# Performance work log

Measured on AMD Instinct MI355X. Metric: run time of the kernel, lower is better.

## Reference

```python
import jax, jax.numpy as jnp
import numpy as np

PI = float(np.pi)
BN_EPS = 1e-3
LN_EPS = 1e-5


def ssslu(x, shape, bias):
    # x * (sin(softsign(x) * shape*pi/2) + (bias + 1))
    s = x / (1.0 + jnp.abs(x))
    return x * (jnp.sin(s * (shape * PI / 2.0)) + (bias + 1.0))


def bn(x, g, b, m, v):
    inv = (g / jnp.sqrt(v + BN_EPS))[None, :, None, None]
    return (x - m[None, :, None, None]) * inv + b[None, :, None, None]


def conv2d(x, w, bias=None, pad=0):
    y = jax.lax.conv_general_dilated(x, w, (1, 1), [(pad, pad), (pad, pad)],
                                     dimension_numbers=('NCHW', 'OIHW', 'NCHW'))
    if bias is not None:
        y = y + bias[None, :, None, None]
    return y


def ln_silu(v):
    # LayerNorm (unit weight, zero bias) over last axis, then SiLU
    mu = jnp.mean(v, axis=-1, keepdims=True)
    var = jnp.mean(jnp.square(v - mu), axis=-1, keepdims=True)
    h = (v - mu) / jnp.sqrt(var + LN_EPS)
    return h * jax.nn.sigmoid(h)


def _forward(x, w_qkv, g_qkv, b_qkv, m_qkv, v_qkv,
             w_co, g_co, b_co, m_co, v_co,
             w_b1, bias_b1, g_b1, b_b1, m_b1, v_b1,
             w_b2, bias_b2, g_b2, b_b2, m_b2, v_b2):
    B, C, H, W = x.shape
    Q = (w_qkv.shape[0] - C) // 2
    # qkv Conv block: conv1x1 -> SSSLU(-3, 0.3) -> BN
    t = bn(ssslu(conv2d(x, w_qkv, pad=0), -3.0, 0.3), g_qkv, b_qkv, m_qkv, v_qkv)
    xq, xk, xv = jnp.split(t, [Q, 2 * Q], axis=1)
    # max-pooled Q/K rows and columns -> [B*Q, W] / [B*Q, H]
    qw = jnp.max(xq, axis=2).reshape(B * Q, W)
    kw = jnp.max(xk, axis=2).reshape(B * Q, W)
    qh = jnp.max(xq, axis=3).reshape(B * Q, H)
    kh = jnp.max(xk, axis=3).reshape(B * Q, H)
    # xaw[i,b] = max_a qw[i,a]*kw[i,b]; xah[i,a] = max_b qh[i,a]*kh[i,b]
    xaw = jnp.max(qw[:, :, None] * kw[:, None, :], axis=1)  # [BQ, W]
    xah = jnp.max(qh[:, :, None] * kh[:, None, :], axis=2)  # [BQ, H]
    xaw = ln_silu(xaw)
    xah = ln_silu(xah)
    xa = (xah[:, :, None] * xaw[:, None, :]).reshape(B, Q, H, W)
    # co: SSSLUConv(Q+C -> Q): conv3x3 -> BN -> SSSLU(1.0, 0)
    xa = jnp.concatenate([xa, xv], axis=1)
    xa = ssslu(bn(conv2d(xa, w_co, pad=1), g_co, b_co, m_co, v_co), 1.0, 0.0)
    # back[0]: Conv(Q -> C, k3, bias): conv -> SSSLU(-3, 0.3) -> BN
    xa = bn(ssslu(conv2d(xa, w_b1, bias_b1, pad=1), -3.0, 0.3), g_b1, b_b1, m_b1, v_b1)
    # back[1]: SSSLUConv(C -> C, k1, bias): conv -> BN -> SSSLU(0.8, 0)
    xa = ssslu(bn(conv2d(xa, w_b2, bias_b2, pad=0), g_b2, b_b2, m_b2, v_b2), 0.8, 0.0)
    # back[2]: Sigmoid; source returns the gate itself
    return jax.nn.sigmoid(xa)


def setup_inputs() -> dict:
    B, C, Q, H, W = 16, 256, 256, 64, 64
    key = jax.random.key(0)
    ks = jax.random.split(key, 32)

    def w_init(k, o, i, kh, kw):
        return jax.random.normal(k, (o, i, kh, kw), jnp.float32) * (1.0 / np.sqrt(i * kh * kw))

    def bn_params(k, c):
        k1, k2, k3, k4 = jax.random.split(k, 4)
        g = jax.random.uniform(k1, (c,), jnp.float32, 0.5, 1.5)
        b = jax.random.normal(k2, (c,), jnp.float32) * 0.1
        m = jax.random.normal(k3, (c,), jnp.float32) * 0.1
        v = jax.random.uniform(k4, (c,), jnp.float32, 0.5, 1.5)
        return g, b, m, v

    x = jax.random.normal(ks[0], (B, C, H, W), jnp.float32)
    w_qkv = w_init(ks[1], 2 * Q + C, C, 1, 1)
    g_qkv, b_qkv, m_qkv, v_qkv = bn_params(ks[2], 2 * Q + C)
    w_co = w_init(ks[3], Q, Q + C, 3, 3)
    g_co, b_co, m_co, v_co = bn_params(ks[4], Q)
    w_b1 = w_init(ks[5], C, Q, 3, 3)
    bias_b1 = jax.random.normal(ks[6], (C,), jnp.float32) * 0.05
    g_b1, b_b1, m_b1, v_b1 = bn_params(ks[7], C)
    w_b2 = w_init(ks[8], C, C, 1, 1)
    bias_b2 = jax.random.normal(ks[9], (C,), jnp.float32) * 0.05
    g_b2, b_b2, m_b2, v_b2 = bn_params(ks[10], C)
    return dict(x=x, w_qkv=w_qkv, g_qkv=g_qkv, b_qkv=b_qkv, m_qkv=m_qkv, v_qkv=v_qkv,
                w_co=w_co, g_co=g_co, b_co=b_co, m_co=m_co, v_co=v_co,
                w_b1=w_b1, bias_b1=bias_b1, g_b1=g_b1, b_b1=b_b1, m_b1=m_b1, v_b1=v_b1,
                w_b2=w_b2, bias_b2=bias_b2, g_b2=g_b2, b_b2=b_b2, m_b2=m_b2, v_b2=v_b2)


def reference(x, w_qkv, g_qkv, b_qkv, m_qkv, v_qkv,
              w_co, g_co, b_co, m_co, v_co,
              w_b1, bias_b1, g_b1, b_b1, m_b1, v_b1,
              w_b2, bias_b2, g_b2, b_b2, m_b2, v_b2):
    return _forward(x, w_qkv, g_qkv, b_qkv, m_qkv, v_qkv,
                    w_co, g_co, b_co, m_co, v_co,
                    w_b1, bias_b1, g_b1, b_b1, m_b1, v_b1,
                    w_b2, bias_b2, g_b2, b_b2, m_b2, v_b2)
```

## Files before the change

### kernel.cpp

```cpp
#include <hip/hip_runtime.h>
#include <hip/hip_bf16.h>
#include <math.h>

#define PI_F 3.14159265358979323846f

typedef unsigned short u16;
typedef unsigned int   u32;
typedef float    f32x4 __attribute__((ext_vector_type(4)));
typedef _Float16 f16x8 __attribute__((ext_vector_type(8)));
typedef u16      u16x8 __attribute__((ext_vector_type(8)));
typedef u16      u16x4 __attribute__((ext_vector_type(4)));

__device__ __forceinline__ u16 f2h(float f){ union{ _Float16 h; u16 u; } c; c.h = (_Float16)f; return c.u; }
__device__ __forceinline__ float h2f(u16 u){ union{ u16 u; _Float16 h; } c; c.u = u; return (float)c.h; }

__device__ __forceinline__ void gl16(const void* g, void* l){
  __builtin_amdgcn_global_load_lds((const __attribute__((address_space(1))) u32*)g,
                                   (__attribute__((address_space(3))) u32*)l, 16, 0, 0);
}

__device__ __forceinline__ int SWZ(int r){ return (r>>1)&3; }

__device__ __forceinline__ float wred_max(float v){
#pragma unroll
  for (int m = 32; m; m >>= 1) v = fmaxf(v, __shfl_xor(v, m));
  return v;
}
__device__ __forceinline__ float wred_min(float v){
#pragma unroll
  for (int m = 32; m; m >>= 1) v = fminf(v, __shfl_xor(v, m));
  return v;
}
__device__ __forceinline__ float wred_sum(float v){
#pragma unroll
  for (int m = 32; m; m >>= 1) v += __shfl_xor(v, m);
  return v;
}

__device__ __forceinline__ float ssslu_f(float x, float shp, float bp1){
  float s = x / (1.0f + fabsf(x));
  return x * (__sinf(s * shp) + bp1);
}

__device__ __forceinline__ float epi_val(float v, float4 p, float shp, float bp1, int ORDER, bool SIG){
  v += p.w;
  if (ORDER == 0){ v = ssslu_f(v, shp, bp1); v = (v - p.z) * p.x + p.y; }
  else           { v = (v - p.z) * p.x + p.y; v = ssslu_f(v, shp, bp1); }
  if (SIG) v = 1.f / (1.f + __expf(-v));
  return v;
}

__device__ __forceinline__ f16x8 mul8h(u16x8 a, u16x8 b){
  union{ u16x8 u; f16x8 h; } A, B; A.u = a; B.u = b;
  return A.h * B.h;
}

__global__ __launch_bounds__(256)
void xpose_k(const float* __restrict__ X, u16* __restrict__ XH)
{
  __shared__ u16 L[16384];
  const int tid = threadIdx.x;
  const int b = blockIdx.x >> 6, h = blockIdx.x & 63;
  const float* xp = X + (size_t)b * 256 * 4096 + h * 64;
#pragma unroll
  for (int i = 0; i < 16; ++i){
    int ci = i * 16 + (tid >> 4);
    int w4 = (tid & 15) * 4;
    float4 v = *(const float4*)(xp + (size_t)ci * 4096 + w4);
    int sw = 4 * ((ci >> 3) & 15);
    u16x4 d;
    d[0] = f2h(v.x); d[1] = f2h(v.y); d[2] = f2h(v.z); d[3] = f2h(v.w);
    *(u16x4*)&L[ci * 64 + (w4 ^ sw)] = d;
  }
  __syncthreads();
  u16* out = XH + (((size_t)b * 4096 + (size_t)h * 64) << 8);
#pragma unroll
  for (int it = 0; it < 8; ++it){
    int w   = it * 8 + (tid >> 5);
    int m   = tid & 31;
    int ci0 = m * 8;
    int base = (w & ~3) ^ (4 * (m & 15));
    int wl   = w & 3;
    u16x8 o;
#pragma unroll
    for (int k = 0; k < 8; ++k)
      o[k] = L[(ci0 + k) * 64 + base + wl];
    *(u16x8*)&out[w * 256 + ci0] = o;
  }
}

template<int CI_T, bool CAT>
__global__ __launch_bounds__(256, 2)
void conv3_mfma(const u16* __restrict__ Apk, const u16* __restrict__ Bg,
                u16* __restrict__ DstH, const float4* __restrict__ pp,
                const u16* __restrict__ xahT_, const u16* __restrict__ xawT_,
                float shp, float bp1, int ORDER)
{
  constexpr int NCC = CI_T / 32;
  constexpr int NIT = NCC * 3;
  __shared__ __align__(16) u16 sAB[37248];

  const int tid  = threadIdx.x;
  const int lane = tid & 63;
  const int wv   = tid >> 6;
  const int wn   = wv;
  const int l15  = lane & 15, l4 = lane >> 4;

  const int bx  = blockIdx.x;
  const int bid = (bx & 7) * 32 + (bx >> 3);
  const int b   = bid >> 4;
  const int r0  = (bid & 15) * 4;
  const int m0  = blockIdx.y * 128;

  if (tid < 192){
    int rr = tid >> 5, rem = tid & 31;
    int wp = (rem & 16) ? 65 : 0;
    *(u32*)&sAB[24576 + rr * 2112 + wp * 32 + (rem & 15) * 2] = 0;
  }
  if (r0 == 0)
    for (int i = tid; i < 1056; i += 256) *(u32*)&sAB[24576 + i * 2] = 0;
  if (r0 == 60)
    for (int i = tid; i < 1056; i += 256) *(u32*)&sAB[24576 + 5 * 2112 + i * 2] = 0;

  const int rA = tid >> 2, s4 = tid & 3;
  const u32 offA0 = ((u32)rA * CI_T + ((s4 ^ SWZ(rA)) << 3)) * 2;
  const u32 offA1 = ((u32)(rA + 64) * CI_T + ((s4 ^ SWZ(rA + 64)) << 3)) * 2;
  const u32 offB  = (((u32)rA << 8) + ((s4 ^ SWZ(rA + 1)) << 3)) * 2;

  auto STAGE_A = [&](int it2){
    int d2 = it2 % 3, c2 = it2 / 3;
    u16* dst = &sAB[(it2 & 1) * 12288 + wv * 512];
    const char* pa = (const char*)(Apk + ((size_t)(d2 * 3 * 256) + m0) * CI_T + c2 * 32);
#pragma unroll
    for (int j2 = 0; j2 < 3; ++j2){
      gl16(pa + offA0, dst + j2 * 4096);
      gl16(pa + offA1, dst + j2 * 4096 + 2048);
      pa += (size_t)256 * CI_T * 2;
    }
  };
  auto STAGE_B = [&](int c2){
#pragma unroll
    for (int j = 0; j < 6; ++j){
      int hh = r0 - 1 + j;
      if ((unsigned)hh >= 64u) continue;
      if (CAT && c2 < 8){
        int w = rA, s = s4;
        int ci0 = c2 * 32 + ((s ^ SWZ(w + 1)) << 3);
        u16x8 vh = *(const u16x8*)&xahT_[((b * 64 + hh) << 8) + ci0];
        u16x8 vw = *(const u16x8*)&xawT_[((b * 64 + w ) << 8) + ci0];
        *(f16x8*)&sAB[24576 + j * 2112 + (w + 1) * 32 + s * 8] = mul8h(vh, vw);
      } else {
        int cio = CAT ? (c2 * 32 - 256) : (c2 * 32);
        const char* pb = (const char*)(Bg + (((size_t)b * 4096 + (size_t)hh * 64) << 8) + cio);
        gl16(pb + offB, &sAB[24576 + j * 2112 + 32 + wv * 512]);
      }
    }
  };

  f32x4 acc[8][4];
#pragma unroll
  for (int i = 0; i < 8; ++i)
#pragma unroll
    for (int j = 0; j < 4; ++j){ acc[i][j][0]=0.f; acc[i][j][1]=0.f; acc[i][j][2]=0.f; acc[i][j][3]=0.f; }

  const char* lds = (const char*)sAB;
  const u32 aoff = (u32)l15 * 64 + (u32)((l4 ^ ((l15 >> 1) & 3)) << 4);
  const char* ab0 = lds + aoff;
  const char* ab1 = lds + aoff + 24576;
  const u32 bcom = 49152u + (u32)wn * 4224;
  const char* bb0 = lds + bcom + (u32)(l15 + 0) * 64 + (u32)((l4 ^ (((l15 + 0) >> 1) & 3)) << 4);
  const char* bb1 = lds + bcom + (u32)(l15 + 1) * 64 + (u32)((l4 ^ (((l15 + 1) >> 1) & 3)) << 4);
  const char* bb2 = lds + bcom + (u32)(l15 + 2) * 64 + (u32)((l4 ^ (((l15 + 2) >> 1) & 3)) << 4);

  STAGE_A(0);

  for (int c = 0; c < NCC; ++c){
#pragma unroll
    for (int d = 0; d < 3; ++d){
      const int it = 3 * c + d;
      if (it + 1 < NIT) STAGE_A(it + 1);
      if (d == 0){ STAGE_B(c); __syncthreads(); }

      const char* ab = ((c + d) & 1) ? ab1 : ab0;
#pragma unroll
      for (int dw = 0; dw < 3; ++dw){
        const char* bp = (dw == 0) ? bb0 : (dw == 1) ? bb1 : bb2;
        f16x8 afr[8], bfr[4];
#pragma unroll
        for (int fm = 0; fm < 8; ++fm)
          afr[fm] = *(const f16x8*)(ab + dw * 8192 + fm * 1024);
#pragma unroll
        for (int fn = 0; fn < 4; ++fn)
          bfr[fn] = *(const f16x8*)(bp + d * 4224 + fn * 1024);
        __builtin_amdgcn_s_setprio(1);
#pragma unroll
        for (int fm = 0; fm < 8; ++fm)
#pragma unroll
          for (int fn = 0; fn < 4; ++fn)
            acc[fm][fn] = __builtin_amdgcn_mfma_f32_16x16x32_f16(afr[fm], bfr[fn], acc[fm][fn], 0, 0, 0);
        __builtin_amdgcn_s_setprio(0);
      }
      __syncthreads();
    }
  }

  const int h = r0 + wn;
#pragma unroll
  for (int fm = 0; fm < 8; ++fm){
    const int cobase = m0 + fm * 16 + 4 * l4;
    float4 P0 = pp[cobase], P1 = pp[cobase+1], P2 = pp[cobase+2], P3 = pp[cobase+3];
#pragma unroll
    for (int fn = 0; fn < 4; ++fn){
      int w = fn * 16 + l15;
      float v0 = epi_val(acc[fm][fn][0], P0, shp, bp1, ORDER, false);
      float v1 = epi_val(acc[fm][fn][1], P1, shp, bp1, ORDER, false);
      float v2 = epi_val(acc[fm][fn][2], P2, shp, bp1, ORDER, false);
      float v3 = epi_val(acc[fm][fn][3], P3, shp, bp1, ORDER, false);
      uint2 st;
      st.x = (u32)f2h(v0) | ((u32)f2h(v1) << 16);
      st.y = (u32)f2h(v2) | ((u32)f2h(v3) << 16);
      *(uint2*)&DstH[(((size_t)b * 4096 + (size_t)h * 64 + w) << 8) + cobase] = st;
    }
  }
}

template<int EPI>
__global__ __launch_bounds__(512, 2)
void conv1_res(const u16* __restrict__ Apk, const u16* __restrict__ Bg,
               u16* __restrict__ DstH, float* __restrict__ DstF,
               const float4* __restrict__ pp,
               float shp, float bp1, int ORDER)
{
  __shared__ __align__(16) u16 AL[65536];

  const int tid  = threadIdx.x;
  const int lane = tid & 63;
  const int wv   = tid >> 6;
  const int wm   = wv >> 2;
  const int wn   = wv & 3;
  const int l15  = lane & 15, l4 = lane >> 4;

  const int bx   = blockIdx.x;
  const int bid  = (bx & 7) * 32 + (bx >> 3);
  const int b    = bid >> 4;
  const int h0   = (bid & 15) * 4;

  {
    const int g0 = tid;
    const int g1 = 512 + tid;
    const int mA0 = g0 >> 2, sA0 = g0 & 3;
    const int mA1 = g1 >> 2, sA1 = g1 & 3;
    const u32 offA0 = ((u32)mA0 * 256 + ((sA0 ^ SWZ(mA0)) << 3)) * 2;
    const u32 offA1 = ((u32)mA1 * 256 + ((sA1 ^ SWZ(mA1)) << 3)) * 2;
#pragma unroll
    for (int c = 0; c < 8; ++c){
      const char* pa = (const char*)(Apk + c * 32);
      gl16(pa + offA0, &AL[c * 8192 + (wv * 64) * 8]);
      gl16(pa + offA1, &AL[c * 8192 + (512 + wv * 64) * 8]);
    }
  }

  const u16* Bp = Bg + (((size_t)b * 4096 + (size_t)(h0 + wn) * 64) << 8) + (l15 << 8) + (l4 << 3);
#define LDB(c, fn) (*(const f16x8*)(Bp + ((fn) * 16 << 8) + (c) * 32))

  f32x4 acc[8][4];
#pragma unroll
  for (int i = 0; i < 8; ++i)
#pragma unroll
    for (int j = 0; j < 4; ++j){ acc[i][j][0]=0.f; acc[i][j][1]=0.f; acc[i][j][2]=0.f; acc[i][j][3]=0.f; }

  f16x8 bn0 = LDB(0, 0), bn1 = LDB(0, 1), bn2 = LDB(0, 2), bn3 = LDB(0, 3);

  __syncthreads();

  const char* abase = (const char*)AL + wm * 8192 + l15 * 64 + ((l4 ^ SWZ(l15)) << 4);

#pragma unroll
  for (int c = 0; c < 8; ++c){
    f16x8 b0 = bn0, b1 = bn1, b2 = bn2, b3 = bn3;
    if (c < 7){
      bn0 = LDB(c + 1, 0); bn1 = LDB(c + 1, 1); bn2 = LDB(c + 1, 2); bn3 = LDB(c + 1, 3);
    }
    f16x8 afr[8];
#pragma unroll
    for (int fm = 0; fm < 8; ++fm)
      afr[fm] = *(const f16x8*)(abase + c * 16384 + fm * 1024);
    __builtin_amdgcn_s_setprio(1);
#pragma unroll
    for (int fm = 0; fm < 8; ++fm){
      acc[fm][0] = __builtin_amdgcn_mfma_f32_16x16x32_f16(afr[fm], b0, acc[fm][0], 0, 0, 0);
      acc[fm][1] = __builtin_amdgcn_mfma_f32_16x16x32_f16(afr[fm], b1, acc[fm][1], 0, 0, 0);
      acc[fm][2] = __builtin_amdgcn_mfma_f32_16x16x32_f16(afr[fm], b2, acc[fm][2], 0, 0, 0);
      acc[fm][3] = __builtin_amdgcn_mfma_f32_16x16x32_f16(afr[fm], b3, acc[fm][3], 0, 0, 0);
    }
    __builtin_amdgcn_s_setprio(0);
  }
#undef LDB

  const int h = h0 + wn;
#pragma unroll
  for (int fm = 0; fm < 8; ++fm){
    const int cobase = wm * 128 + fm * 16 + 4 * l4;
    float4 P0 = pp[cobase], P1 = pp[cobase+1], P2 = pp[cobase+2], P3 = pp[cobase+3];
#pragma unroll
    for (int fn = 0; fn < 4; ++fn){
      int w = fn * 16 + l15;
      if (EPI == 1){
        float v0 = epi_val(acc[fm][fn][0], P0, shp, bp1, ORDER, false);
        float v1 = epi_val(acc[fm][fn][1], P1, shp, bp1, ORDER, false);
        float v2 = epi_val(acc[fm][fn][2], P2, shp, bp1, ORDER, false);
        float v3 = epi_val(acc[fm][fn][3], P3, shp, bp1, ORDER, false);
        uint2 st;
        st.x = (u32)f2h(v0) | ((u32)f2h(v1) << 16);
        st.y = (u32)f2h(v2) | ((u32)f2h(v3) << 16);
        *(uint2*)&DstH[(((size_t)b * 4096 + (size_t)h * 64 + w) << 8) + cobase] = st;
      } else {
        float v0 = epi_val(acc[fm][fn][0], P0, shp, bp1, ORDER, true);
        float v1 = epi_val(acc[fm][fn][1], P1, shp, bp1, ORDER, true);
        float v2 = epi_val(acc[fm][fn][2], P2, shp, bp1, ORDER, true);
        float v3 = epi_val(acc[fm][fn][3], P3, shp, bp1, ORDER, true);
        size_t base = ((size_t)(b * 256 + cobase)) * 4096 + (size_t)h * 64 + w;
        DstF[base]          = v0;
        DstF[base + 4096]   = v1;
        DstF[base + 2*4096] = v2;
        DstF[base + 3*4096] = v3;
      }
    }
  }
}

__global__ __launch_bounds__(256)
void poolh_k(const u16* __restrict__ T, float* __restrict__ rowp)
{
  __shared__ float L[8][256];
  const int tid = threadIdx.x;
  const int b = blockIdx.x >> 6, h = blockIdx.x & 63;
  const int wg = tid >> 5;
  const int c8 = (tid & 31) * 8;
  const u16* base = T + (((size_t)b * 4096 + (size_t)h * 64) << 8) + c8;
  float m[8];
#pragma unroll
  for (int e = 0; e < 8; ++e) m[e] = -3.0e38f;
#pragma unroll
  for (int j = 0; j < 8; ++j){
    u16x8 v = *(const u16x8*)(base + ((wg * 8 + j) << 8));
#pragma unroll
    for (int e = 0; e < 8; ++e) m[e] = fmaxf(m[e], h2f(v[e]));
  }
#pragma unroll
  for (int e = 0; e < 8; ++e) L[wg][c8 + e] = m[e];
  __syncthreads();
  const int c = tid;
  float r = L[0][c];
#pragma unroll
  for (int g = 1; g < 8; ++g) r = fmaxf(r, L[g][c]);
  rowp[(((b << 8) | c) << 6) + h] = r;
}

__global__ __launch_bounds__(256)
void poolw_k(const u16* __restrict__ T, float* __restrict__ colp)
{
  __shared__ float L[4][256];
  const int tid = threadIdx.x;
  const int b = blockIdx.x >> 6, w = blockIdx.x & 63;
  const int hs = tid >> 6;
  const int c4 = (tid & 63) * 4;
  const u16* base = T + (((size_t)b * 4096 + w) << 8) + c4;
  float m0 = -3.0e38f, m1 = -3.0e38f, m2 = -3.0e38f, m3 = -3.0e38f;
#pragma unroll
  for (int hi = 0; hi < 16; ++hi){
    int h = hi * 4 + hs;
    u16x4 v = *(const u16x4*)(base + ((size_t)h << 14));
    m0 = fmaxf(m0, h2f(v[0]));
    m1 = fmaxf(m1, h2f(v[1]));
    m2 = fmaxf(m2, h2f(v[2]));
    m3 = fmaxf(m3, h2f(v[3]));
  }
  L[hs][c4 + 0] = m0; L[hs][c4 + 1] = m1; L[hs][c4 + 2] = m2; L[hs][c4 + 3] = m3;
  __syncthreads();
  const int c = tid;
  float r = fmaxf(fmaxf(L[0][c], L[1][c]), fmaxf(L[2][c], L[3][c]));
  colp[(((b << 8) | c) << 6) + w] = r;
}

__device__ __forceinline__ float ln_silu_wave(float v){
  float mu = wred_sum(v) * (1.f / 64.f);
  float d = v - mu;
  float var = wred_sum(d * d) * (1.f / 64.f);
  float hn = d * rsqrtf(var + 1e-5f);
  return hn / (1.f + __expf(-hn));
}

__global__ void attn_k(const float* __restrict__ qw, const float* __restrict__ kw,
                       const float* __restrict__ qh, const float* __restrict__ kh,
                       u16* __restrict__ xahT, u16* __restrict__ xawT)
{
  int row  = blockIdx.x * 4 + (threadIdx.x >> 6);
  int lane = threadIdx.x & 63;
  int idx  = (row << 6) + lane;
  float qwv = qw[idx], kwv = kw[idx], qhv = qh[idx], khv = kh[idx];
  float Pq = wred_max(qwv), mq = wred_min(qwv);
  float Pk = wred_max(khv), mk = wred_min(khv);
  float aw = fmaxf(kwv * Pq, kwv * mq);
  float ah = fmaxf(qhv * Pk, qhv * mk);
  aw = ln_silu_wave(aw);
  ah = ln_silu_wave(ah);
  int b = row >> 8, q = row & 255;
  xawT[((b * 64 + lane) << 8) + q] = f2h(aw);
  xahT[((b * 64 + lane) << 8) + q] = f2h(ah);
}

__global__ void pack_k(const float* __restrict__ wqkv, const float* __restrict__ wco,
                       const float* __restrict__ wb1, const float* __restrict__ wb2,
                       const float* gq, const float* bq, const float* mq, const float* vq,
                       const float* gc, const float* bc, const float* mc, const float* vc,
                       const float* g1, const float* b1, const float* m1, const float* v1, const float* bias1,
                       const float* g2, const float* b2, const float* m2, const float* v2, const float* bias2,
                       u16* __restrict__ WQ, u16* __restrict__ WCO, u16* __restrict__ WB1, u16* __restrict__ WB2,
                       float4* __restrict__ PP)
{
  const int E0 = 196608, E1 = 196608 + 1179648, E2 = 196608 + 1179648 + 589824, E3 = 2031616;
  int i = blockIdx.x * 256 + threadIdx.x;
  if (i >= E3 + 1536) return;
  if (i < E0){ WQ[i] = f2h(wqkv[i]); }
  else if (i < E1){
    int d = i - E0; int tap = d / 131072; int rm = d % 131072; int m = rm >> 9; int ci = rm & 511;
    WCO[d] = f2h(wco[(size_t)((m << 9) | ci) * 9 + tap]);
  } else if (i < E2){
    int d = i - E1; int tap = d / 65536; int rm = d & 65535; int m = rm >> 8; int ci = rm & 255;
    WB1[d] = f2h(wb1[(size_t)((m << 8) | ci) * 9 + tap]);
  } else if (i < E3){
    int d = i - E2; WB2[d] = f2h(wb2[d]);
  } else {
    int c = i - E3;
    float g, be, mm, vv, bi;
    if (c < 768){ g = gq[c]; be = bq[c]; mm = mq[c]; vv = vq[c]; bi = 0.f; }
    else if (c < 1024){ int j = c - 768;  g = gc[j]; be = bc[j]; mm = mc[j]; vv = vc[j]; bi = 0.f; }
    else if (c < 1280){ int j = c - 1024; g = g1[j]; be = b1[j]; mm = m1[j]; vv = v1[j]; bi = bias1[j]; }
    else              { int j = c - 1280; g = g2[j]; be = b2[j]; mm = m2[j]; vv = v2[j]; bi = bias2[j]; }
    PP[c] = make_float4(g / sqrtf(vv + 1e-3f), be, mm, bi);
  }
}

extern "C" void kernel_launch(void* const* d_in, const int* in_sizes, int n_in,
                              void* d_out, int out_size, void* d_ws, size_t ws_size,
                              hipStream_t stream)
{
  const float* x       = (const float*)d_in[0];
  const float* w_qkv   = (const float*)d_in[1];
  const float* g_qkv   = (const float*)d_in[2];
  const float* b_qkv   = (const float*)d_in[3];
  const float* m_qkv   = (const float*)d_in[4];
  const float* v_qkv   = (const float*)d_in[5];
  const float* w_co    = (const float*)d_in[6];
  const float* g_co    = (const float*)d_in[7];
  const float* b_co    = (const float*)d_in[8];
  const float* m_co    = (const float*)d_in[9];
  const float* v_co    = (const float*)d_in[10];
  const float* w_b1    = (const float*)d_in[11];
  const float* bias_b1 = (const float*)d_in[12];
  const float* g_b1    = (const float*)d_in[13];
  const float* b_b1    = (const float*)d_in[14];
  const float* m_b1    = (const float*)d_in[15];
  const float* v_b1    = (const float*)d_in[16];
  const float* w_b2    = (const float*)d_in[17];
  const float* bias_b2 = (const float*)d_in[18];
  const float* g_b2    = (const float*)d_in[19];
  const float* b_b2    = (const float*)d_in[20];
  const float* m_b2    = (const float*)d_in[21];
  const float* v_b2    = (const float*)d_in[22];
  float* out = (float*)d_out;

  char* W = (char*)d_ws;
  u16*    WQ   = (u16*)(W + 0);
  u16*    WCO  = (u16*)(W + 393216);
  u16*    WB1  = (u16*)(W + 2752512);
  u16*    WB2  = (u16*)(W + 3932160);
  float4* PP   = (float4*)(W + 4063232);
  u16*    TQK  = (u16*)(W + 4087808);
  u16*    TV   = TQK;
  u16*    XAHT = (u16*)(W + 37642240);
  u16*    XAWT = (u16*)(W + 38166528);
  u16*    XH   = (u16*)(W + 38690816);
  u16*    Y1   = (u16*)(W + 38690816);
  u16*    Y2   = TV;
  float*  qh_  = (float*)(W + 72245248);
  float*  kh_  = (float*)(W + 73293824);
  float*  qw_  = (float*)(W + 74342400);
  float*  kw_  = (float*)(W + 75390976);

  const size_t NEED = 76439552;
  if (ws_size < NEED) return;

  const float SHP_N3 = -3.0f * PI_F * 0.5f;
  const float SHP_1  =  1.0f * PI_F * 0.5f;
  const float SHP_08 =  0.8f * PI_F * 0.5f;

  dim3 blk(256);

  pack_k<<<7942, blk, 0, stream>>>(w_qkv, w_co, w_b1, w_b2,
      g_qkv, b_qkv, m_qkv, v_qkv,
      g_co,  b_co,  m_co,  v_co,
      g_b1,  b_b1,  m_b1,  v_b1,  bias_b1,
      g_b2,  b_b2,  m_b2,  v_b2,  bias_b2,
      WQ, WCO, WB1, WB2, PP);

  xpose_k<<<1024, blk, 0, stream>>>(x, XH);

  conv1_res<1><<<256, 512, 0, stream>>>(
      WQ, XH, TQK, nullptr, PP, SHP_N3, 1.3f, 0);
  poolh_k<<<1024, blk, 0, stream>>>(TQK, qh_);
  poolw_k<<<1024, blk, 0, stream>>>(TQK, qw_);

  conv1_res<1><<<256, 512, 0, stream>>>(
      WQ + (size_t)256 * 256, XH, TQK, nullptr, PP + 256, SHP_N3, 1.3f, 0);
  poolh_k<<<1024, blk, 0, stream>>>(TQK, kh_);
  poolw_k<<<1024, blk, 0, stream>>>(TQK, kw_);

  attn_k<<<1024, blk, 0, stream>>>(qw_, kw_, qh_, kh_, XAHT, XAWT);

  conv1_res<1><<<256, 512, 0, stream>>>(
      WQ + (size_t)512 * 256, XH, TV, nullptr, PP + 512, SHP_N3, 1.3f, 0);

  conv3_mfma<512, true><<<dim3(256, 2), blk, 0, stream>>>(
      WCO, TV, Y1, PP + 768, XAHT, XAWT, SHP_1, 1.0f, 1);

  conv3_mfma<256, false><<<dim3(256, 2), blk, 0, stream>>>(
      WB1, Y1, Y2, PP + 1024, nullptr, nullptr, SHP_N3, 1.3f, 0);

  conv1_res<2><<<256, 512, 0, stream>>>(
      WB2, Y2, nullptr, out, PP + 1280, SHP_08, 1.0f, 1);
}
```

Measured before the change: 376.9 us.

## Enlarge conv3x3 tile to two rows per wave, double-buffer B, fuse pooling kernels

The 3x3 conv kernel now computes 8 output rows per block (2 per wave) with double-buffered B staging, so each A fragment feeds twice as many MFMAs and the B load overlaps compute. This halves the grid, raises LDS use, and drops to one block per CU, which can cut occupancy. The separate row/column max-pool kernels are merged into one pass that uses float atomic max for column maxima, after an init kernel fills the buffers. The atomics add contention, and a single init covering both q and k buffers is assumed.

```diff
diff --git a/kernel.cpp b/kernel.cpp
--- a/kernel.cpp
+++ b/kernel.cpp
@@ -48,6 +48,11 @@
   else           { v = (v - p.z) * p.x + p.y; v = ssslu_f(v, shp, bp1); }
   if (SIG) v = 1.f / (1.f + __expf(-v));
   return v;
+}
+
+__device__ __forceinline__ void atomicMaxF(float* a, float v){
+  if (v >= 0.f) atomicMax(reinterpret_cast<int*>(a), __float_as_int(v));
+  else          atomicMin(reinterpret_cast<unsigned int*>(a), __float_as_uint(v));
 }
 
 __device__ __forceinline__ f16x8 mul8h(u16x8 a, u16x8 b){
@@ -90,7 +95,7 @@
 }
 
 template<int CI_T, bool CAT>
-__global__ __launch_bounds__(256, 2)
+__global__ __launch_bounds__(256, 1)
 void conv3_mfma(const u16* __restrict__ Apk, const u16* __restrict__ Bg,
                 u16* __restrict__ DstH, const float4* __restrict__ pp,
                 const u16* __restrict__ xahT_, const u16* __restrict__ xawT_,
@@ -98,29 +103,35 @@
 {
   constexpr int NCC = CI_T / 32;
   constexpr int NIT = NCC * 3;
-  __shared__ __align__(16) u16 sAB[37248];
+  __shared__ __align__(16) u16 sAB[66816];
 
   const int tid  = threadIdx.x;
   const int lane = tid & 63;
   const int wv   = tid >> 6;
-  const int wn   = wv;
   const int l15  = lane & 15, l4 = lane >> 4;
 
   const int bx  = blockIdx.x;
-  const int bid = (bx & 7) * 32 + (bx >> 3);
-  const int b   = bid >> 4;
-  const int r0  = (bid & 15) * 4;
+  const int bid = (bx & 7) * 16 + (bx >> 3);
+  const int b   = bid >> 3;
+  const int r0  = (bid & 7) * 8;
   const int m0  = blockIdx.y * 128;
 
-  if (tid < 192){
-    int rr = tid >> 5, rem = tid & 31;
+  for (int i = tid; i < 640; i += 256){
+    int bu = i >> 5;
+    int rem = i & 31;
     int wp = (rem & 16) ? 65 : 0;
-    *(u32*)&sAB[24576 + rr * 2112 + wp * 32 + (rem & 15) * 2] = 0;
+    *(u32*)&sAB[24576 + bu * 2112 + wp * 32 + (rem & 15) * 2] = 0;
   }
   if (r0 == 0)
-    for (int i = tid; i < 1056; i += 256) *(u32*)&sAB[24576 + i * 2] = 0;
-  if (r0 == 60)
-    for (int i = tid; i < 1056; i += 256) *(u32*)&sAB[24576 + 5 * 2112 + i * 2] = 0;
+    for (int i = tid; i < 1056; i += 256){
+      *(u32*)&sAB[24576 + i * 2] = 0;
+      *(u32*)&sAB[24576 + 21120 + i * 2] = 0;
+    }
+  if (r0 == 56)
+    for (int i = tid; i < 1056; i += 256){
+      *(u32*)&sAB[24576 + 9 * 2112 + i * 2] = 0;
+      *(u32*)&sAB[24576 + 21120 + 9 * 2112 + i * 2] = 0;
+    }
 
   const int rA = tid >> 2, s4 = tid & 3;
   const u32 offA0 = ((u32)rA * CI_T + ((s4 ^ SWZ(rA)) << 3)) * 2;
@@ -139,8 +150,9 @@
     }
   };
   auto STAGE_B = [&](int c2){
-#pragma unroll
-    for (int j = 0; j < 6; ++j){
+    const int bb = 24576 + (c2 & 1) * 21120;
+#pragma unroll
+    for (int j = 0; j < 10; ++j){
       int hh = r0 - 1 + j;
       if ((unsigned)hh >= 64u) continue;
       if (CAT && c2 < 8){
@@ -148,78 +160,99 @@
         int ci0 = c2 * 32 + ((s ^ SWZ(w + 1)) << 3);
         u16x8 vh = *(const u16x8*)&xahT_[((b * 64 + hh) << 8) + ci0];
         u16x8 vw = *(const u16x8*)&xawT_[((b * 64 + w ) << 8) + ci0];
-        *(f16x8*)&sAB[24576 + j * 2112 + (w + 1) * 32 + s * 8] = mul8h(vh, vw);
+        *(f16x8*)&sAB[bb + j * 2112 + (w + 1) * 32 + s * 8] = mul8h(vh, vw);
       } else {
         int cio = CAT ? (c2 * 32 - 256) : (c2 * 32);
         const char* pb = (const char*)(Bg + (((size_t)b * 4096 + (size_t)hh * 64) << 8) + cio);
-        gl16(pb + offB, &sAB[24576 + j * 2112 + 32 + wv * 512]);
+        gl16(pb + offB, &sAB[bb + j * 2112 + 32 + wv * 512]);
       }
     }
   };
 
-  f32x4 acc[8][4];
+  f32x4 acc0[8][4], acc1[8][4];
 #pragma unroll
   for (int i = 0; i < 8; ++i)
 #pragma unroll
-    for (int j = 0; j < 4; ++j){ acc[i][j][0]=0.f; acc[i][j][1]=0.f; acc[i][j][2]=0.f; acc[i][j][3]=0.f; }
+    for (int j = 0; j < 4; ++j){
+      acc0[i][j][0]=0.f; acc0[i][j][1]=0.f; acc0[i][j][2]=0.f; acc0[i][j][3]=0.f;
+      acc1[i][j][0]=0.f; acc1[i][j][1]=0.f; acc1[i][j][2]=0.f; acc1[i][j][3]=0.f;
+    }
 
   const char* lds = (const char*)sAB;
   const u32 aoff = (u32)l15 * 64 + (u32)((l4 ^ ((l15 >> 1) & 3)) << 4);
   const char* ab0 = lds + aoff;
   const char* ab1 = lds + aoff + 24576;
-  const u32 bcom = 49152u + (u32)wn * 4224;
-  const char* bb0 = lds + bcom + (u32)(l15 + 0) * 64 + (u32)((l4 ^ (((l15 + 0) >> 1) & 3)) << 4);
-  const char* bb1 = lds + bcom + (u32)(l15 + 1) * 64 + (u32)((l4 ^ (((l15 + 1) >> 1) & 3)) << 4);
-  const char* bb2 = lds + bcom + (u32)(l15 + 2) * 64 + (u32)((l4 ^ (((l15 + 2) >> 1) & 3)) << 4);
+  const u32 brow0 = 49152u + (u32)(2 * wv + 0) * 4224;
+  const u32 brow1 = 49152u + (u32)(2 * wv + 1) * 4224;
+#define BSW(dw) ((u32)(l15 + (dw)) * 64 + (u32)((l4 ^ (((l15 + (dw)) >> 1) & 3)) << 4))
+  const char* ba0 = lds + brow0 + BSW(0);
+  const char* ba1 = lds + brow0 + BSW(1);
+  const char* ba2 = lds + brow0 + BSW(2);
+  const char* bc0 = lds + brow1 + BSW(0);
+  const char* bc1 = lds + brow1 + BSW(1);
+  const char* bc2 = lds + brow1 + BSW(2);
+#undef BSW
 
   STAGE_A(0);
+  STAGE_B(0);
+  __syncthreads();
 
   for (int c = 0; c < NCC; ++c){
+    const u32 bofs = (c & 1) ? 42240u : 0u;
 #pragma unroll
     for (int d = 0; d < 3; ++d){
       const int it = 3 * c + d;
       if (it + 1 < NIT) STAGE_A(it + 1);
-      if (d == 0){ STAGE_B(c); __syncthreads(); }
+      if (d == 0 && c + 1 < NCC) STAGE_B(c + 1);
 
       const char* ab = ((c + d) & 1) ? ab1 : ab0;
 #pragma unroll
       for (int dw = 0; dw < 3; ++dw){
-        const char* bp = (dw == 0) ? bb0 : (dw == 1) ? bb1 : bb2;
-        f16x8 afr[8], bfr[4];
+        const char* p0 = ((dw == 0) ? ba0 : (dw == 1) ? ba1 : ba2) + bofs + d * 4224;
+        const char* p1 = ((dw == 0) ? bc0 : (dw == 1) ? bc1 : bc2) + bofs + d * 4224;
+        f16x8 afr[8], b0r[4], b1r[4];
 #pragma unroll
         for (int fm = 0; fm < 8; ++fm)
           afr[fm] = *(const f16x8*)(ab + dw * 8192 + fm * 1024);
 #pragma unroll
-        for (int fn = 0; fn < 4; ++fn)
-          bfr[fn] = *(const f16x8*)(bp + d * 4224 + fn * 1024);
+        for (int fn = 0; fn < 4; ++fn){
+          b0r[fn] = *(const f16x8*)(p0 + fn * 1024);
+          b1r[fn] = *(const f16x8*)(p1 + fn * 1024);
+        }
         __builtin_amdgcn_s_setprio(1);
 #pragma unroll
         for (int fm = 0; fm < 8; ++fm)
 #pragma unroll
-          for (int fn = 0; fn < 4; ++fn)
-            acc[fm][fn] = __builtin_amdgcn_mfma_f32_16x16x32_f16(afr[fm], bfr[fn], acc[fm][fn], 0, 0, 0);
+          for (int fn = 0; fn < 4; ++fn){
+            acc0[fm][fn] = __builtin_amdgcn_mfma_f32_16x16x32_f16(afr[fm], b0r[fn], acc0[fm][fn], 0, 0, 0);
+            acc1[fm][fn] = __builtin_amdgcn_mfma_f32_16x16x32_f16(afr[fm], b1r[fn], acc1[fm][fn], 0, 0, 0);
+          }
         __builtin_amdgcn_s_setprio(0);
       }
       __syncthreads();
     }
   }
 
-  const int h = r0 + wn;
-#pragma unroll
-  for (int fm = 0; fm < 8; ++fm){
-    const int cobase = m0 + fm * 16 + 4 * l4;
-    float4 P0 = pp[cobase], P1 = pp[cobase+1], P2 = pp[cobase+2], P3 = pp[cobase+3];
-#pragma unroll
-    for (int fn = 0; fn < 4; ++fn){
-      int w = fn * 16 + l15;
-      float v0 = epi_val(acc[fm][fn][0], P0, shp, bp1, ORDER, false);
-      float v1 = epi_val(acc[fm][fn][1], P1, shp, bp1, ORDER, false);
-      float v2 = epi_val(acc[fm][fn][2], P2, shp, bp1, ORDER, false);
-      float v3 = epi_val(acc[fm][fn][3], P3, shp, bp1, ORDER, false);
-      uint2 st;
-      st.x = (u32)f2h(v0) | ((u32)f2h(v1) << 16);
-      st.y = (u32)f2h(v2) | ((u32)f2h(v3) << 16);
-      *(uint2*)&DstH[(((size_t)b * 4096 + (size_t)h * 64 + w) << 8) + cobase] = st;
+#pragma unroll
+  for (int rr = 0; rr < 2; ++rr){
+    const int h = r0 + 2 * wv + rr;
+#pragma unroll
+    for (int fm = 0; fm < 8; ++fm){
+      const int cobase = m0 + fm * 16 + 4 * l4;
+      float4 P0 = pp[cobase], P1 = pp[cobase+1], P2 = pp[cobase+2], P3 = pp[cobase+3];
+#pragma unroll
+      for (int fn = 0; fn < 4; ++fn){
+        int w = fn * 16 + l15;
+        f32x4 a = rr ? acc1[fm][fn] : acc0[fm][fn];
+        float v0 = epi_val(a[0], P0, shp, bp1, ORDER, false);
+        float v1 = epi_val(a[1], P1, shp, bp1, ORDER, false);
+        float v2 = epi_val(a[2], P2, shp, bp1, ORDER, false);
+        float v3 = epi_val(a[3], P3, shp, bp1, ORDER, false);
+        uint2 st;
+        st.x = (u32)f2h(v0) | ((u32)f2h(v1) << 16);
+        st.y = (u32)f2h(v2) | ((u32)f2h(v3) << 16);
+        *(uint2*)&DstH[(((size_t)b * 4096 + (size_t)h * 64 + w) << 8) + cobase] = st;
+      }
     }
   }
 }
@@ -330,57 +363,57 @@
 }
 
 __global__ __launch_bounds__(256)
-void poolh_k(const u16* __restrict__ T, float* __restrict__ rowp)
+void pool2_k(const u16* __restrict__ T, float* __restrict__ rowp, float* __restrict__ colp)
 {
   __shared__ float L[8][256];
   const int tid = threadIdx.x;
-  const int b = blockIdx.x >> 6, h = blockIdx.x & 63;
+  const int b = blockIdx.x >> 4, hq = blockIdx.x & 15;
   const int wg = tid >> 5;
   const int c8 = (tid & 31) * 8;
-  const u16* base = T + (((size_t)b * 4096 + (size_t)h * 64) << 8) + c8;
-  float m[8];
-#pragma unroll
-  for (int e = 0; e < 8; ++e) m[e] = -3.0e38f;
-#pragma unroll
-  for (int j = 0; j < 8; ++j){
-    u16x8 v = *(const u16x8*)(base + ((wg * 8 + j) << 8));
-#pragma unroll
-    for (int e = 0; e < 8; ++e) m[e] = fmaxf(m[e], h2f(v[e]));
-  }
-#pragma unroll
-  for (int e = 0; e < 8; ++e) L[wg][c8 + e] = m[e];
-  __syncthreads();
-  const int c = tid;
-  float r = L[0][c];
-#pragma unroll
-  for (int g = 1; g < 8; ++g) r = fmaxf(r, L[g][c]);
-  rowp[(((b << 8) | c) << 6) + h] = r;
-}
-
-__global__ __launch_bounds__(256)
-void poolw_k(const u16* __restrict__ T, float* __restrict__ colp)
-{
-  __shared__ float L[4][256];
-  const int tid = threadIdx.x;
-  const int b = blockIdx.x >> 6, w = blockIdx.x & 63;
-  const int hs = tid >> 6;
-  const int c4 = (tid & 63) * 4;
-  const u16* base = T + (((size_t)b * 4096 + w) << 8) + c4;
-  float m0 = -3.0e38f, m1 = -3.0e38f, m2 = -3.0e38f, m3 = -3.0e38f;
-#pragma unroll
-  for (int hi = 0; hi < 16; ++hi){
-    int h = hi * 4 + hs;
-    u16x4 v = *(const u16x4*)(base + ((size_t)h << 14));
-    m0 = fmaxf(m0, h2f(v[0]));
-    m1 = fmaxf(m1, h2f(v[1]));
-    m2 = fmaxf(m2, h2f(v[2]));
-    m3 = fmaxf(m3, h2f(v[3]));
-  }
-  L[hs][c4 + 0] = m0; L[hs][c4 + 1] = m1; L[hs][c4 + 2] = m2; L[hs][c4 + 3] = m3;
-  __syncthreads();
-  const int c = tid;
-  float r = fmaxf(fmaxf(L[0][c], L[1][c]), fmaxf(L[2][c], L[3][c]));
-  colp[(((b << 8) | c) << 6) + w] = r;
+  float cp[8][8];
+#pragma unroll
+  for (int j = 0; j < 8; ++j)
+#pragma unroll
+    for (int e = 0; e < 8; ++e) cp[j][e] = -3.0e38f;
+
+#pragma unroll
+  for (int hi = 0; hi < 4; ++hi){
+    const int h = hq * 4 + hi;
+    const u16* base = T + (((size_t)b * 4096 + (size_t)h * 64) << 8) + c8;
+    float m[8];
+#pragma unroll
+    for (int e = 0; e < 8; ++e) m[e] = -3.0e38f;
+#pragma unroll
+    for (int j = 0; j < 8; ++j){
+      u16x8 v = *(const u16x8*)(base + ((wg * 8 + j) << 8));
+#pragma unroll
+      for (int e = 0; e < 8; ++e){
+        float f = h2f(v[e]);
+        m[e] = fmaxf(m[e], f);
+        cp[j][e] = fmaxf(cp[j][e], f);
+      }
+    }
+#pragma unroll
+    for (int e = 0; e < 8; ++e) L[wg][c8 + e] = m[e];
+    __syncthreads();
+    float r = L[0][tid];
+#pragma unroll
+    for (int g = 1; g < 8; ++g) r = fmaxf(r, L[g][tid]);
+    rowp[(((b << 8) | tid) << 6) + h] = r;
+    __syncthreads();
+  }
+#pragma unroll
+  for (int e = 0; e < 8; ++e)
+#pragma unroll
+    for (int j = 0; j < 8; ++j)
+      atomicMaxF(&colp[(((b << 8) | (c8 + e)) << 6) + wg * 8 + j], cp[j][e]);
+}
+
+__global__ void initpool_k(float* __restrict__ p)
+{
+  int i = blockIdx.x * 1024 + threadIdx.x * 4;
+  float4 v = make_float4(-3.0e38f, -3.0e38f, -3.0e38f, -3.0e38f);
+  *(float4*)(p + i) = v;
 }
 
 __device__ __forceinline__ float ln_silu_wave(float v){
@@ -507,25 +540,25 @@
 
   xpose_k<<<1024, blk, 0, stream>>>(x, XH);
 
+  initpool_k<<<512, blk, 0, stream>>>(qw_);
+
   conv1_res<1><<<256, 512, 0, stream>>>(
       WQ, XH, TQK, nullptr, PP, SHP_N3, 1.3f, 0);
-  poolh_k<<<1024, blk, 0, stream>>>(TQK, qh_);
-  poolw_k<<<1024, blk, 0, stream>>>(TQK, qw_);
+  pool2_k<<<256, blk, 0, stream>>>(TQK, qh_, qw_);
 
   conv1_res<1><<<256, 512, 0, stream>>>(
       WQ + (size_t)256 * 256, XH, TQK, nullptr, PP + 256, SHP_N3, 1.3f, 0);
-  poolh_k<<<1024, blk, 0, stream>>>(TQK, kh_);
-  poolw_k<<<1024, blk, 0, stream>>>(TQK, kw_);
+  pool2_k<<<256, blk, 0, stream>>>(TQK, kh_, kw_);
 
   attn_k<<<1024, blk, 0, stream>>>(qw_, kw_, qh_, kh_, XAHT, XAWT);
 
   conv1_res<1><<<256, 512, 0, stream>>>(
       WQ + (size_t)512 * 256, XH, TV, nullptr, PP + 512, SHP_N3, 1.3f, 0);
 
-  conv3_mfma<512, true><<<dim3(256, 2), blk, 0, stream>>>(
+  conv3_mfma<512, true><<<dim3(128, 2), blk, 0, stream>>>(
       WCO, TV, Y1, PP + 768, XAHT, XAWT, SHP_1, 1.0f, 1);
 
-  conv3_mfma<256, false><<<dim3(256, 2), blk, 0, stream>>>(
+  conv3_mfma<256, false><<<dim3(128, 2), blk, 0, stream>>>(
       WB1, Y1, Y2, PP + 1024, nullptr, nullptr, SHP_N3, 1.3f, 0);
 
   conv1_res<2><<<256, 512, 0, stream>>>(
```

After: 608.2 us. 61.4% more time.

## Register-prefetch B tiles one step ahead in conv and 1x1 GEMM kernels

Applied to the files above, without the earlier changes.

The 3x3 conv kernel's B-tile staging now loads global data into registers one channel chunk ahead and writes it to LDS in the next iteration, replacing direct global-to-LDS loads. This aims to hide global latency behind MFMA work. The 1x1 GEMM kernel moves from one-deep to two-deep register prefetch of B fragments, with loads issued after each step's MFMAs. Both raise register pressure, which may lower occupancy, and the LDS write layout changes to a linear per-thread index.

```diff
diff --git a/kernel.cpp b/kernel.cpp
--- a/kernel.cpp
+++ b/kernel.cpp
@@ -138,21 +138,36 @@
       pa += (size_t)256 * CI_T * 2;
     }
   };
-  auto STAGE_B = [&](int c2){
+
+  u16x8 br[6];
+  auto LOADB = [&](int c2){
+    if (CAT && c2 < 8) return;
+    int cio = CAT ? (c2 * 32 - 256) : (c2 * 32);
 #pragma unroll
     for (int j = 0; j < 6; ++j){
       int hh = r0 - 1 + j;
       if ((unsigned)hh >= 64u) continue;
-      if (CAT && c2 < 8){
-        int w = rA, s = s4;
-        int ci0 = c2 * 32 + ((s ^ SWZ(w + 1)) << 3);
+      const char* pb = (const char*)(Bg + (((size_t)b * 4096 + (size_t)hh * 64) << 8) + cio);
+      br[j] = *(const u16x8*)(pb + offB);
+    }
+  };
+  auto WRITEB = [&](int c2){
+    if (CAT && c2 < 8){
+#pragma unroll
+      for (int j = 0; j < 6; ++j){
+        int hh = r0 - 1 + j;
+        if ((unsigned)hh >= 64u) continue;
+        int ci0 = c2 * 32 + ((s4 ^ SWZ(rA + 1)) << 3);
         u16x8 vh = *(const u16x8*)&xahT_[((b * 64 + hh) << 8) + ci0];
-        u16x8 vw = *(const u16x8*)&xawT_[((b * 64 + w ) << 8) + ci0];
-        *(f16x8*)&sAB[24576 + j * 2112 + (w + 1) * 32 + s * 8] = mul8h(vh, vw);
-      } else {
-        int cio = CAT ? (c2 * 32 - 256) : (c2 * 32);
-        const char* pb = (const char*)(Bg + (((size_t)b * 4096 + (size_t)hh * 64) << 8) + cio);
-        gl16(pb + offB, &sAB[24576 + j * 2112 + 32 + wv * 512]);
+        u16x8 vw = *(const u16x8*)&xawT_[((b * 64 + rA) << 8) + ci0];
+        *(f16x8*)&sAB[24576 + j * 2112 + 32 + 8 * tid] = mul8h(vh, vw);
+      }
+    } else {
+#pragma unroll
+      for (int j = 0; j < 6; ++j){
+        int hh = r0 - 1 + j;
+        if ((unsigned)hh >= 64u) continue;
+        *(u16x8*)&sAB[24576 + j * 2112 + 32 + 8 * tid] = br[j];
       }
     }
   };
@@ -173,13 +188,18 @@
   const char* bb2 = lds + bcom + (u32)(l15 + 2) * 64 + (u32)((l4 ^ (((l15 + 2) >> 1) & 3)) << 4);
 
   STAGE_A(0);
+  LOADB(0);
 
   for (int c = 0; c < NCC; ++c){
 #pragma unroll
     for (int d = 0; d < 3; ++d){
       const int it = 3 * c + d;
       if (it + 1 < NIT) STAGE_A(it + 1);
-      if (d == 0){ STAGE_B(c); __syncthreads(); }
+      if (d == 0){
+        WRITEB(c);
+        if (c + 1 < NCC) LOADB(c + 1);
+        __syncthreads();
+      }
 
       const char* ab = ((c + d) & 1) ? ab1 : ab0;
 #pragma unroll
@@ -269,7 +289,11 @@
 #pragma unroll
     for (int j = 0; j < 4; ++j){ acc[i][j][0]=0.f; acc[i][j][1]=0.f; acc[i][j][2]=0.f; acc[i][j][3]=0.f; }
 
-  f16x8 bn0 = LDB(0, 0), bn1 = LDB(0, 1), bn2 = LDB(0, 2), bn3 = LDB(0, 3);
+  f16x8 bq[2][4];
+#pragma unroll
+  for (int fn = 0; fn < 4; ++fn) bq[0][fn] = LDB(0, fn);
+#pragma unroll
+  for (int fn = 0; fn < 4; ++fn) bq[1][fn] = LDB(1, fn);
 
   __syncthreads();
 
@@ -277,10 +301,6 @@
 
 #pragma unroll
   for (int c = 0; c < 8; ++c){
-    f16x8 b0 = bn0, b1 = bn1, b2 = bn2, b3 = bn3;
-    if (c < 7){
-      bn0 = LDB(c + 1, 0); bn1 = LDB(c + 1, 1); bn2 = LDB(c + 1, 2); bn3 = LDB(c + 1, 3);
-    }
     f16x8 afr[8];
 #pragma unroll
     for (int fm = 0; fm < 8; ++fm)
@@ -288,12 +308,16 @@
     __builtin_amdgcn_s_setprio(1);
 #pragma unroll
     for (int fm = 0; fm < 8; ++fm){
-      acc[fm][0] = __builtin_amdgcn_mfma_f32_16x16x32_f16(afr[fm], b0, acc[fm][0], 0, 0, 0);
-      acc[fm][1] = __builtin_amdgcn_mfma_f32_16x16x32_f16(afr[fm], b1, acc[fm][1], 0, 0, 0);
-      acc[fm][2] = __builtin_amdgcn_mfma_f32_16x16x32_f16(afr[fm], b2, acc[fm][2], 0, 0, 0);
-      acc[fm][3] = __builtin_amdgcn_mfma_f32_16x16x32_f16(afr[fm], b3, acc[fm][3], 0, 0, 0);
+      acc[fm][0] = __builtin_amdgcn_mfma_f32_16x16x32_f16(afr[fm], bq[c & 1][0], acc[fm][0], 0, 0, 0);
+      acc[fm][1] = __builtin_amdgcn_mfma_f32_16x16x32_f16(afr[fm], bq[c & 1][1], acc[fm][1], 0, 0, 0);
+      acc[fm][2] = __builtin_amdgcn_mfma_f32_16x16x32_f16(afr[fm], bq[c & 1][2], acc[fm][2], 0, 0, 0);
+      acc[fm][3] = __builtin_amdgcn_mfma_f32_16x16x32_f16(afr[fm], bq[c & 1][3], acc[fm][3], 0, 0, 0);
     }
     __builtin_amdgcn_s_setprio(0);
+    if (c + 2 < 8){
+#pragma unroll
+      for (int fn = 0; fn < 4; ++fn) bq[c & 1][fn] = LDB(c + 2, fn);
+    }
   }
 #undef LDB
 
```

After: 391.9 us. +4.0%, slower.
